# Kernel tuning notes

Measured on AMD Instinct MI355X. Metric: run time of the kernel, lower is better.

## Reference

```python
import jax, jax.numpy as jnp
import numpy as np

N = 50000   # nodes
E = 600000  # edges
D = 128     # emb_dim
L = 3       # num_layers
G = 500     # graphs in batch
AV = 128    # atom feature vocab per column (9 columns)
BV = 8      # bond feature vocab per column (3 columns)


def setup_inputs() -> dict:
    key = jax.random.key(0)
    ks = jax.random.split(key, 16)
    r = lambda k, sh: jax.random.normal(k, sh, jnp.float32) * 0.02
    return dict(
        x=jax.random.randint(ks[0], (N, 9), 0, AV),
        edge_index=jax.random.randint(ks[1], (2, E), 0, N),
        edge_attr=jax.random.randint(ks[2], (E, 3), 0, BV),
        batch=(jnp.arange(N) * G) // N,  # sorted node->graph map, covers all G graphs
        atom_emb=r(ks[3], (9, AV, D)),
        bond_emb=r(ks[4], (L, 3, BV, D)),  # per-layer BondEncoder
        eps=jnp.zeros((L,), jnp.float32),
        conv_w1=r(ks[5], (L, D, 2 * D)), conv_b1=jnp.zeros((L, 2 * D), jnp.float32),
        conv_bn_g=jnp.ones((L, 2 * D), jnp.float32), conv_bn_b=jnp.zeros((L, 2 * D), jnp.float32),
        conv_w2=r(ks[6], (L, 2 * D, D)), conv_b2=jnp.zeros((L, D), jnp.float32),
        bn_g=jnp.ones((L, D), jnp.float32), bn_b=jnp.zeros((L, D), jnp.float32),
        vn_emb=jnp.zeros((1, D), jnp.float32),  # init constant 0, as in torch code
        vn_w1=r(ks[7], (L - 1, D, 2 * D)), vn_b1=jnp.zeros((L - 1, 2 * D), jnp.float32),
        vn_bn1_g=jnp.ones((L - 1, 2 * D), jnp.float32), vn_bn1_b=jnp.zeros((L - 1, 2 * D), jnp.float32),
        vn_w2=r(ks[8], (L - 1, 2 * D, D)), vn_b2=jnp.zeros((L - 1, D), jnp.float32),
        vn_bn2_g=jnp.ones((L - 1, D), jnp.float32), vn_bn2_b=jnp.zeros((L - 1, D), jnp.float32),
    )


def _bn(h, g, b):
    # BatchNorm1d, training-mode batch statistics (biased var), eps=1e-5
    mu = h.mean(0)
    var = h.var(0)
    return (h - mu) * jax.lax.rsqrt(var + 1e-5) * g + b


def reference(x, edge_index, edge_attr, batch, atom_emb, bond_emb, eps,
              conv_w1, conv_b1, conv_bn_g, conv_bn_b, conv_w2, conv_b2,
              bn_g, bn_b, vn_emb, vn_w1, vn_b1, vn_bn1_g, vn_bn1_b,
              vn_w2, vn_b2, vn_bn2_g, vn_bn2_b):
    src, dst = edge_index[0], edge_index[1]
    # AtomEncoder: sum of per-column embeddings -> [N, D]
    h = sum(atom_emb[i][x[:, i]] for i in range(9))
    vn = jnp.broadcast_to(vn_emb[0], (G, D))  # virtualnode_embedding(zeros(G))
    for l in range(L):
        h = h + vn[batch]                                   # virtual-node broadcast
        ee = sum(bond_emb[l, i][edge_attr[:, i]] for i in range(3))  # BondEncoder [E, D]
        msg = jax.nn.relu(h[src] + ee)                      # message: relu(x_j + edge_attr)
        agg = jax.ops.segment_sum(msg, dst, num_segments=N)  # aggr='add'
        t = (1.0 + eps[l]) * h + agg
        t = _bn(t @ conv_w1[l] + conv_b1[l], conv_bn_g[l], conv_bn_b[l])
        t = jax.nn.relu(t) @ conv_w2[l] + conv_b2[l]
        hn = _bn(t, bn_g[l], bn_b[l])                       # outer batch_norms[layer]
        if l < L - 1:
            hn = jax.nn.relu(hn)                            # relu before dropout (non-final)
            # virtual node update: global_add_pool(h_list[layer]) + vn -> MLP
            vt = jax.ops.segment_sum(h, batch, num_segments=G) + vn
            vt = jax.nn.relu(_bn(vt @ vn_w1[l] + vn_b1[l], vn_bn1_g[l], vn_bn1_b[l]))
            vn = jax.nn.relu(_bn(vt @ vn_w2[l] + vn_b2[l], vn_bn2_g[l], vn_bn2_b[l]))
        h = hn
    return h
```

## Files before the change

### kernel.cpp

```cpp
#include <hip/hip_runtime.h>

#define DEV __global__ __launch_bounds__(256)

constexpr int NN = 50000;
constexpr int NE = 600000;
constexpr int D  = 128;
constexpr int NG = 500;
constexpr int NL = 3;
constexpr int SCAN_B = 512;
constexpr int NBLK = (NN + SCAN_B - 1) / SCAN_B;

typedef __attribute__((ext_vector_type(8))) short bf16x8;
typedef __attribute__((ext_vector_type(4))) float f32x4;

__device__ inline ushort f2bf(float f) {
  unsigned u = __builtin_bit_cast(unsigned, f);
  unsigned r = u + 0x7FFFu + ((u >> 16) & 1u);
  return (ushort)(r >> 16);
}
__device__ inline float bf2f(ushort h) {
  unsigned u = ((unsigned)h) << 16;
  return __builtin_bit_cast(float, u);
}


DEV void k_atom(const int* __restrict__ x, const float* __restrict__ emb,
                const float* __restrict__ vne, float* __restrict__ hv) {
  int t = blockIdx.x * 256 + threadIdx.x;
  int n = t >> 5, c = (t & 31) * 4;
  if (n >= NN) return;
  float4 acc = *(const float4*)(vne + c);
  #pragma unroll
  for (int i = 0; i < 9; ++i) {
    int v = x[n * 9 + i];
    float4 e = *(const float4*)(emb + ((size_t)(i * 128 + v)) * D + c);
    acc.x += e.x; acc.y += e.y; acc.z += e.z; acc.w += e.w;
  }
  *(float4*)(hv + (size_t)n * D + c) = acc;
}

DEV void k_vninit(const float* __restrict__ src, float* __restrict__ vn) {
  int t = blockIdx.x * 256 + threadIdx.x;
  int g = t >> 5, c = (t & 31) * 4;
  if (g >= NG) return;
  *(float4*)(vn + (size_t)g * D + c) = *(const float4*)(src + c);
}

DEV void k_post(const float* __restrict__ z, const float* __restrict__ sum,
                const float* __restrict__ sq, const float* __restrict__ gam,
                const float* __restrict__ bet, float invM,
                const float* __restrict__ vnadd, const int* __restrict__ batch,
                float* __restrict__ dst, int M, int relu) {
  int t = blockIdx.x * 256 + threadIdx.x;
  int n = t >> 5, c = (t & 31) * 4;
  if (n >= M) return;
  f32x4 s = *(const f32x4*)(sum + c);
  f32x4 q = *(const f32x4*)(sq + c);
  f32x4 g = *(const f32x4*)(gam + c);
  f32x4 b = *(const f32x4*)(bet + c);
  f32x4 v = *(const f32x4*)(z + (size_t)n * 128 + c);
  f32x4 o;
  #pragma unroll
  for (int j = 0; j < 4; ++j) {
    float mu = s[j] * invM;
    float var = q[j] * invM - mu * mu;
    float sc = g[j] * rsqrtf(var + 1e-5f);
    float sh = b[j] - mu * sc;
    o[j] = fmaf(v[j], sc, sh);
    if (relu) o[j] = fmaxf(o[j], 0.f);
  }
  if (vnadd) {
    f32x4 a = *(const f32x4*)(vnadd + (size_t)batch[n] * 128 + c);
    #pragma unroll
    for (int j = 0; j < 4; ++j) o[j] += a[j];
  }
  *(f32x4*)(dst + (size_t)n * 128 + c) = o;
}


DEV void k_hist(const int* __restrict__ ei, int* __restrict__ cnt) {
  int e = blockIdx.x * 256 + threadIdx.x;
  if (e < NE) atomicAdd(&cnt[ei[NE + e]], 1);
}

__global__ __launch_bounds__(SCAN_B) void k_scan_a(const int* __restrict__ cnt,
                                                   int* __restrict__ rowptr,
                                                   int* __restrict__ bsum) {
  __shared__ int sh[SCAN_B];
  int i = blockIdx.x * SCAN_B + threadIdx.x;
  int v = (i < NN) ? cnt[i] : 0;
  sh[threadIdx.x] = v;
  __syncthreads();
  for (int off = 1; off < SCAN_B; off <<= 1) {
    int u = (threadIdx.x >= (unsigned)off) ? sh[threadIdx.x - off] : 0;
    __syncthreads();
    sh[threadIdx.x] += u;
    __syncthreads();
  }
  if (i < NN) rowptr[i + 1] = sh[threadIdx.x];
  if (threadIdx.x == SCAN_B - 1) bsum[blockIdx.x] = sh[SCAN_B - 1];
}

__global__ void k_scan_b(int* __restrict__ bsum, int nb) {
  if (threadIdx.x == 0 && blockIdx.x == 0) {
    int acc = 0;
    for (int i = 0; i < nb; ++i) { int v = bsum[i]; bsum[i] = acc; acc += v; }
  }
}

__global__ __launch_bounds__(SCAN_B) void k_scan_c(int* __restrict__ rowptr,
                                                   const int* __restrict__ bsum) {
  int i = blockIdx.x * SCAN_B + threadIdx.x;
  if (i < NN) rowptr[i + 1] += bsum[blockIdx.x];
  if (i == 0) rowptr[0] = 0;
}

DEV void k_fill(const int* __restrict__ ei, const int* __restrict__ eattr,
                int* __restrict__ cursor, unsigned* __restrict__ csr) {
  int e = blockIdx.x * 256 + threadIdx.x;
  if (e >= NE) return;
  int dn = ei[NE + e];
  int p = atomicAdd(&cursor[dn], 1);
  unsigned a0 = (unsigned)eattr[e * 3 + 0];
  unsigned a1 = (unsigned)eattr[e * 3 + 1];
  unsigned a2 = (unsigned)eattr[e * 3 + 2];
  csr[p] = (unsigned)ei[e] | (a0 << 17) | (a1 << 20) | (a2 << 23);
}


DEV void k_agg(const float* __restrict__ hv, const unsigned* __restrict__ csr,
               const int* __restrict__ rowptr, const float* __restrict__ bond,
               const float* __restrict__ epsp, unsigned* __restrict__ Ahi,
               unsigned* __restrict__ Alo) {
  __shared__ float eb[3 * 8 * D];
  for (int i = threadIdx.x; i < 3 * 8 * D; i += 256) eb[i] = bond[i];
  __syncthreads();
  int wid = (blockIdx.x * 256 + threadIdx.x) >> 6;
  int lane = threadIdx.x & 63;
  if (wid >= NN) return;
  int d0 = lane * 2;
  float ax = 0.f, ay = 0.f;
  int p = rowptr[wid];
  const int p1 = rowptr[wid + 1];
  for (; p + 4 <= p1; p += 4) {
    unsigned pk[4];
    #pragma unroll
    for (int j = 0; j < 4; ++j) pk[j] = csr[p + j];
    float2 hvv[4];
    #pragma unroll
    for (int j = 0; j < 4; ++j)
      hvv[j] = *(const float2*)(hv + (size_t)(pk[j] & 0x1FFFF) * D + d0);
    #pragma unroll
    for (int j = 0; j < 4; ++j) {
      float2 e0 = *(const float2*)(eb + (((pk[j] >> 17) & 7u)) * D + d0);
      float2 e1 = *(const float2*)(eb + (8 + ((pk[j] >> 20) & 7u)) * D + d0);
      float2 e2 = *(const float2*)(eb + (16 + ((pk[j] >> 23) & 7u)) * D + d0);
      ax += fmaxf(hvv[j].x + e0.x + e1.x + e2.x, 0.f);
      ay += fmaxf(hvv[j].y + e0.y + e1.y + e2.y, 0.f);
    }
  }
  for (; p < p1; ++p) {
    unsigned pk = csr[p];
    float2 hvv = *(const float2*)(hv + (size_t)(pk & 0x1FFFF) * D + d0);
    float2 e0 = *(const float2*)(eb + (((pk >> 17) & 7u)) * D + d0);
    float2 e1 = *(const float2*)(eb + (8 + ((pk >> 20) & 7u)) * D + d0);
    float2 e2 = *(const float2*)(eb + (16 + ((pk >> 23) & 7u)) * D + d0);
    ax += fmaxf(hvv.x + e0.x + e1.x + e2.x, 0.f);
    ay += fmaxf(hvv.y + e0.y + e1.y + e2.y, 0.f);
  }
  float2 hvo = *(const float2*)(hv + (size_t)wid * D + d0);
  float ef = 1.f + epsp[0];
  float a0 = fmaf(ef, hvo.x, ax);
  float a1 = fmaf(ef, hvo.y, ay);
  ushort h0 = f2bf(a0), h1 = f2bf(a1);
  ushort l0 = f2bf(a0 - bf2f(h0)), l1 = f2bf(a1 - bf2f(h1));
  Ahi[(size_t)wid * 64 + lane] = (unsigned)h0 | ((unsigned)h1 << 16);
  Alo[(size_t)wid * 64 + lane] = (unsigned)l0 | ((unsigned)l1 << 16);
}

__global__ __launch_bounds__(256) void k_cvtw(const float* __restrict__ src, int K,
                                              int lognc, ushort* __restrict__ th,
                                              ushort* __restrict__ tl) {
  int NC = 1 << lognc;
  size_t base = (size_t)blockIdx.y * K * NC;
  int i = blockIdx.x * 256 + threadIdx.x;
  if (i >= K * NC) return;
  int k = i >> lognc, c = i & (NC - 1);
  float v = src[base + i];
  ushort hi = f2bf(v);
  th[base + (size_t)c * K + k] = hi;
  tl[base + (size_t)c * K + k] = f2bf(v - bf2f(hi));
}

template <int AMODE, int COLS, int NT, bool ATOMIC>
__global__ __launch_bounds__(NT) void k_mgemm(
    int M, int K, const float* __restrict__ A0, const ushort* __restrict__ Ath,
    const ushort* __restrict__ Atl, const float* __restrict__ bnsum,
    const float* __restrict__ bnsq, const float* __restrict__ bngam,
    const float* __restrict__ bnbet, float invPrevM,
    const ushort* __restrict__ Wth, const ushort* __restrict__ Wtl,
    const float* __restrict__ bias, float* __restrict__ Y,
    float* __restrict__ colsum, float* __restrict__ colsq,
    float* __restrict__ partial) {
  constexpr int NWC = COLS / 64;
  __shared__ __align__(16) ushort Ah[4][128][8];
  __shared__ __align__(16) ushort Al[4][128][8];
  __shared__ __align__(16) ushort Bh[4][COLS][8];
  __shared__ __align__(16) ushort Bl[4][COLS][8];
  __shared__ float bnsc[AMODE == 2 ? 256 : 1];
  __shared__ float bnsh[AMODE == 2 ? 256 : 1];
  const int tid = threadIdx.x;
  const int row0 = blockIdx.x * 128;
  const int lane = tid & 63, w = tid >> 6;
  const int wr = w / NWC, wc = w % NWC;
  const int kc = lane >> 4, lr = lane & 15;

  if (AMODE == 2) {
    for (int c = tid; c < K; c += NT) {
      float mu = bnsum[c] * invPrevM;
      float var = bnsq[c] * invPrevM - mu * mu;
      float sc = bngam[c] * rsqrtf(var + 1e-5f);
      bnsc[c] = sc;
      bnsh[c] = bnbet[c] - mu * sc;
    }
    __syncthreads();
  }

  f32x4 acc[4][4] = {};

  for (int k0 = 0; k0 < K; k0 += 32) {
    for (int i = tid; i < 512; i += NT) {
      const int c = i >> 7, r = i & 127;
      const int gk = k0 + c * 8;
      const int gr = row0 + r;
      if (AMODE == 3) {
        uint4 vh = make_uint4(0, 0, 0, 0), vl = make_uint4(0, 0, 0, 0);
        if (gr < M) {
          vh = *(const uint4*)(Ath + (size_t)gr * K + gk);
          vl = *(const uint4*)(Atl + (size_t)gr * K + gk);
        }
        *(uint4*)&Ah[c][r][0] = vh;
        *(uint4*)&Al[c][r][0] = vl;
      } else {
        float v[8];
        if (gr < M) {
          f32x4 a0 = *(const f32x4*)(A0 + (size_t)gr * K + gk);
          f32x4 a1 = *(const f32x4*)(A0 + (size_t)gr * K + gk + 4);
          if (AMODE == 2) {
            f32x4 s0 = *(const f32x4*)&bnsc[gk];
            f32x4 s1 = *(const f32x4*)&bnsc[gk + 4];
            f32x4 t0 = *(const f32x4*)&bnsh[gk];
            f32x4 t1 = *(const f32x4*)&bnsh[gk + 4];
            #pragma unroll
            for (int j = 0; j < 4; ++j) {
              v[j] = fmaxf(fmaf(a0[j], s0[j], t0[j]), 0.f);
              v[4 + j] = fmaxf(fmaf(a1[j], s1[j], t1[j]), 0.f);
            }
          } else {
            #pragma unroll
            for (int j = 0; j < 4; ++j) { v[j] = a0[j]; v[4 + j] = a1[j]; }
          }
        } else {
          #pragma unroll
          for (int j = 0; j < 8; ++j) v[j] = 0.f;
        }
        alignas(16) ushort th[8], tl[8];
        #pragma unroll
        for (int j = 0; j < 8; ++j) {
          ushort hi = f2bf(v[j]);
          th[j] = hi;
          tl[j] = f2bf(v[j] - bf2f(hi));
        }
        *(uint4*)&Ah[c][r][0] = *(const uint4*)th;
        *(uint4*)&Al[c][r][0] = *(const uint4*)tl;
      }
    }
    for (int i = tid; i < COLS * 4; i += NT) {
      const int c = i / COLS, r = i % COLS;
      const int gk = k0 + c * 8;
      *(uint4*)&Bh[c][r][0] = *(const uint4*)(Wth + (size_t)r * K + gk);
      *(uint4*)&Bl[c][r][0] = *(const uint4*)(Wtl + (size_t)r * K + gk);
    }
    __syncthreads();
    bf16x8 bhf[4], blf[4];
    #pragma unroll
    for (int fc = 0; fc < 4; ++fc) {
      bhf[fc] = *(const bf16x8*)&Bh[kc][wc * 64 + fc * 16 + lr][0];
      blf[fc] = *(const bf16x8*)&Bl[kc][wc * 64 + fc * 16 + lr][0];
    }
    #pragma unroll
    for (int fr = 0; fr < 4; ++fr) {
      bf16x8 ahf = *(const bf16x8*)&Ah[kc][wr * 64 + fr * 16 + lr][0];
      bf16x8 alf = *(const bf16x8*)&Al[kc][wr * 64 + fr * 16 + lr][0];
      #pragma unroll
      for (int fc = 0; fc < 4; ++fc) {
        acc[fr][fc] = __builtin_amdgcn_mfma_f32_16x16x32_bf16(ahf, bhf[fc], acc[fr][fc], 0, 0, 0);
        acc[fr][fc] = __builtin_amdgcn_mfma_f32_16x16x32_bf16(alf, bhf[fc], acc[fr][fc], 0, 0, 0);
        acc[fr][fc] = __builtin_amdgcn_mfma_f32_16x16x32_bf16(ahf, blf[fc], acc[fr][fc], 0, 0, 0);
      }
    }
    __syncthreads();
  }

  float* sred = reinterpret_cast<float*>(&Ah[0][0][0]);
  float* qred = sred + 2 * COLS;
  #pragma unroll
  for (int fc = 0; fc < 4; ++fc) {
    const int gc = wc * 64 + fc * 16 + lr;
    const float bb = bias[gc];
    float cs = 0.f, cq = 0.f;
    #pragma unroll
    for (int fr = 0; fr < 4; ++fr) {
      const int rb = row0 + wr * 64 + fr * 16 + kc * 4;
      #pragma unroll
      for (int rg = 0; rg < 4; ++rg) {
        int gr = rb + rg;
        if (gr < M) {
          float v = acc[fr][fc][rg] + bb;
          Y[(size_t)gr * COLS + gc] = v;
          cs += v;
          cq += v * v;
        }
      }
    }
    cs += __shfl_xor(cs, 16); cs += __shfl_xor(cs, 32);
    cq += __shfl_xor(cq, 16); cq += __shfl_xor(cq, 32);
    if (kc == 0) {
      sred[wr * COLS + gc] = cs;
      qred[wr * COLS + gc] = cq;
    }
  }
  __syncthreads();
  for (int c = tid; c < COLS; c += NT) {
    float s = sred[c] + sred[COLS + c];
    float q = qred[c] + qred[COLS + c];
    if (ATOMIC) {
      atomicAdd(&colsum[c], s);
      atomicAdd(&colsq[c], q);
    } else {
      partial[(size_t)blockIdx.x * 2 * COLS + c] = s;
      partial[(size_t)blockIdx.x * 2 * COLS + COLS + c] = q;
    }
  }
}

__global__ __launch_bounds__(256) void k_red(const float* __restrict__ part, int nb,
                                             int width, float* __restrict__ outSum,
                                             float* __restrict__ outSq) {
  const int j = blockIdx.x;
  float a = 0.f;
  for (int b = threadIdx.x; b < nb; b += 256)
    a += part[(size_t)b * 2 * width + j];
  a += __shfl_xor(a, 1);  a += __shfl_xor(a, 2);  a += __shfl_xor(a, 4);
  a += __shfl_xor(a, 8);  a += __shfl_xor(a, 16); a += __shfl_xor(a, 32);
  __shared__ float red[4];
  const int lane = threadIdx.x & 63, wv = threadIdx.x >> 6;
  if (lane == 0) red[wv] = a;
  __syncthreads();
  if (threadIdx.x == 0) {
    float s = red[0] + red[1] + red[2] + red[3];
    if (j < width) outSum[j] = s;
    else outSq[j - width] = s;
  }
}


DEV void k_pool(const float* __restrict__ hv, const int* __restrict__ batch,
                const float* __restrict__ vn, float* __restrict__ vt) {
  int g = blockIdx.x;
  int lo = 0, hi = NN;
  while (lo < hi) { int mid = (lo + hi) >> 1; if (batch[mid] < g) lo = mid + 1; else hi = mid; }
  int s = lo;
  hi = NN;
  while (lo < hi) { int mid = (lo + hi) >> 1; if (batch[mid] < g + 1) lo = mid + 1; else hi = mid; }
  int e = lo;
  int ry = threadIdx.x >> 5, cx = threadIdx.x & 31;
  float4 acc = make_float4(0.f, 0.f, 0.f, 0.f);
  for (int n = s + ry; n < e; n += 8) {
    float4 v = *(const float4*)(hv + (size_t)n * D + cx * 4);
    acc.x += v.x; acc.y += v.y; acc.z += v.z; acc.w += v.w;
  }
  __shared__ float4 red[8][32];
  red[ry][cx] = acc;
  __syncthreads();
  for (int st = 4; st >= 1; st >>= 1) {
    if (ry < st) {
      float4 o = red[ry + st][cx];
      red[ry][cx].x += o.x; red[ry][cx].y += o.y;
      red[ry][cx].z += o.z; red[ry][cx].w += o.w;
    }
    __syncthreads();
  }
  if (ry == 0) {
    float4 v = red[0][cx];
    float4 b = *(const float4*)(vn + (size_t)g * D + cx * 4);
    v.x += b.x; v.y += b.y; v.z += b.z; v.w += b.w;
    *(float4*)(vt + (size_t)g * D + cx * 4) = v;
  }
}


extern "C" void kernel_launch(void* const* d_in, const int* in_sizes, int n_in,
                              void* d_out, int out_size, void* d_ws, size_t ws_size,
                              hipStream_t stream) {
  const int* x = (const int*)d_in[0];
  const int* ei = (const int*)d_in[1];
  const int* eattr = (const int*)d_in[2];
  const int* batch = (const int*)d_in[3];
  const float* atom_emb = (const float*)d_in[4];
  const float* bond_emb = (const float*)d_in[5];
  const float* eps = (const float*)d_in[6];
  const float* conv_w1 = (const float*)d_in[7];
  const float* conv_b1 = (const float*)d_in[8];
  const float* conv_bn_g = (const float*)d_in[9];
  const float* conv_bn_b = (const float*)d_in[10];
  const float* conv_w2 = (const float*)d_in[11];
  const float* conv_b2 = (const float*)d_in[12];
  const float* bn_g = (const float*)d_in[13];
  const float* bn_b = (const float*)d_in[14];
  const float* vn_emb = (const float*)d_in[15];
  const float* vn_w1 = (const float*)d_in[16];
  const float* vn_b1 = (const float*)d_in[17];
  const float* vn_bn1_g = (const float*)d_in[18];
  const float* vn_bn1_b = (const float*)d_in[19];
  const float* vn_w2 = (const float*)d_in[20];
  const float* vn_b2 = (const float*)d_in[21];
  const float* vn_bn2_g = (const float*)d_in[22];
  const float* vn_bn2_b = (const float*)d_in[23];
  float* out = (float*)d_out;

  char* w = (char*)d_ws;
  auto alloc = [&](size_t bytes) {
    char* p = w;
    w += (bytes + 255) & ~((size_t)255);
    return p;
  };
  float* h   = (float*)alloc((size_t)NN * D * 4);
  float* hv  = (float*)alloc((size_t)NN * D * 4);
  float* y   = (float*)alloc((size_t)NN * 256 * 4);
  unsigned* Ahi = (unsigned*)alloc((size_t)NN * 64 * 4);
  unsigned* Alo = (unsigned*)alloc((size_t)NN * 64 * 4);
  float* vn  = (float*)alloc((size_t)NG * D * 4);
  float* vt  = (float*)alloc((size_t)NG * D * 4);
  float* yv  = (float*)alloc((size_t)NG * 256 * 4);
  float* zv  = (float*)alloc((size_t)NG * D * 4);
  float* stats = (float*)alloc(16 * 512 * 4);
  auto SUM = [&](int slot) { return stats + slot * 512; };
  auto SQ  = [&](int slot) { return stats + slot * 512 + 256; };
  const int gx = (NN + 127) / 128;
  const int gv = (NG + 127) / 128;
  float* partA = (float*)alloc((size_t)gx * 512 * 4);
  float* partB = (float*)alloc((size_t)gx * 256 * 4);
  int* cnt = (int*)alloc((size_t)NN * 4);
  int* rowptr = (int*)alloc((size_t)(NN + 1) * 4);
  int* cursor = (int*)alloc((size_t)NN * 4);
  unsigned* csr = (unsigned*)alloc((size_t)NE * 4);
  int* bsum = (int*)alloc(128 * 4);
  ushort* wt1h = (ushort*)alloc((size_t)NL * 256 * 128 * 2);
  ushort* wt1l = (ushort*)alloc((size_t)NL * 256 * 128 * 2);
  ushort* wt2h = (ushort*)alloc((size_t)NL * 128 * 256 * 2);
  ushort* wt2l = (ushort*)alloc((size_t)NL * 128 * 256 * 2);
  ushort* vw1h = (ushort*)alloc((size_t)2 * 256 * 128 * 2);
  ushort* vw1l = (ushort*)alloc((size_t)2 * 256 * 128 * 2);
  ushort* vw2h = (ushort*)alloc((size_t)2 * 128 * 256 * 2);
  ushort* vw2l = (ushort*)alloc((size_t)2 * 128 * 256 * 2);

  hipMemsetAsync(stats, 0, 16 * 512 * 4, stream);

  k_cvtw<<<dim3(128, NL), 256, 0, stream>>>(conv_w1, 128, 8, wt1h, wt1l);
  k_cvtw<<<dim3(128, NL), 256, 0, stream>>>(conv_w2, 256, 7, wt2h, wt2l);
  k_cvtw<<<dim3(128, 2), 256, 0, stream>>>(vn_w1, 128, 8, vw1h, vw1l);
  k_cvtw<<<dim3(128, 2), 256, 0, stream>>>(vn_w2, 256, 7, vw2h, vw2l);

  k_atom<<<(NN * 32 + 255) / 256, 256, 0, stream>>>(x, atom_emb, vn_emb, hv);
  k_vninit<<<(NG * 32 + 255) / 256, 256, 0, stream>>>(vn_emb, vn);

  hipMemsetAsync(cnt, 0, (size_t)NN * 4, stream);
  k_hist<<<(NE + 255) / 256, 256, 0, stream>>>(ei, cnt);
  k_scan_a<<<NBLK, SCAN_B, 0, stream>>>(cnt, rowptr, bsum);
  k_scan_b<<<1, 64, 0, stream>>>(bsum, NBLK);
  k_scan_c<<<NBLK, SCAN_B, 0, stream>>>(rowptr, bsum);
  hipMemcpyAsync(cursor, rowptr, (size_t)NN * 4, hipMemcpyDeviceToDevice, stream);
  k_fill<<<(NE + 255) / 256, 256, 0, stream>>>(ei, eattr, cursor, csr);

  for (int l = 0; l < NL; ++l) {
    const int sc1 = l, sc2 = 3 + l, sv1 = 6 + l, sv2 = 8 + l;
    k_agg<<<(NN * 64 + 255) / 256, 256, 0, stream>>>(
        hv, csr, rowptr, bond_emb + (size_t)l * 3 * 8 * D, eps + l, Ahi, Alo);

    k_mgemm<3, 256, 512, false><<<gx, 512, 0, stream>>>(
        NN, 128, nullptr, (const ushort*)Ahi, (const ushort*)Alo,
        nullptr, nullptr, nullptr, nullptr, 0.f,
        wt1h + (size_t)l * 256 * 128, wt1l + (size_t)l * 256 * 128,
        conv_b1 + l * 256, y, nullptr, nullptr, partA);
    k_red<<<512, 256, 0, stream>>>(partA, gx, 256, SUM(sc1), SQ(sc1));
    k_mgemm<2, 128, 256, false><<<gx, 256, 0, stream>>>(
        NN, 256, y, nullptr, nullptr, SUM(sc1), SQ(sc1),
        conv_bn_g + l * 256, conv_bn_b + l * 256, 1.f / NN,
        wt2h + (size_t)l * 128 * 256, wt2l + (size_t)l * 128 * 256,
        conv_b2 + l * 128, h, nullptr, nullptr, partB);
    k_red<<<256, 256, 0, stream>>>(partB, gx, 128, SUM(sc2), SQ(sc2));

    if (l < NL - 1) {
      k_pool<<<NG, 256, 0, stream>>>(hv, batch, vn, vt);
      k_mgemm<0, 256, 512, true><<<gv, 512, 0, stream>>>(
          NG, 128, vt, nullptr, nullptr, nullptr, nullptr, nullptr, nullptr, 0.f,
          vw1h + (size_t)l * 256 * 128, vw1l + (size_t)l * 256 * 128,
          vn_b1 + l * 256, yv, SUM(sv1), SQ(sv1), nullptr);
      k_mgemm<2, 128, 256, true><<<gv, 256, 0, stream>>>(
          NG, 256, yv, nullptr, nullptr, SUM(sv1), SQ(sv1),
          vn_bn1_g + l * 256, vn_bn1_b + l * 256, 1.f / NG,
          vw2h + (size_t)l * 128 * 256, vw2l + (size_t)l * 128 * 256,
          vn_b2 + l * 128, zv, SUM(sv2), SQ(sv2), nullptr);
      k_post<<<(NG * 32 + 255) / 256, 256, 0, stream>>>(
          zv, SUM(sv2), SQ(sv2), vn_bn2_g + l * 128, vn_bn2_b + l * 128,
          1.f / NG, nullptr, nullptr, vn, NG, 1);
      k_post<<<(NN * 32 + 255) / 256, 256, 0, stream>>>(
          h, SUM(sc2), SQ(sc2), bn_g + l * 128, bn_b + l * 128,
          1.f / NN, vn, batch, hv, NN, 1);
    } else {
      k_post<<<(NN * 32 + 255) / 256, 256, 0, stream>>>(
          h, SUM(sc2), SQ(sc2), bn_g + l * 128, bn_b + l * 128,
          1.f / NN, nullptr, nullptr, out, NN, 0);
    }
  }
}
```

Measured before the change: 824.5 us.

## Store first GEMM output in bf16 and merge small setup kernels

```diff
diff --git a/kernel.cpp b/kernel.cpp
--- a/kernel.cpp
+++ b/kernel.cpp
@@ -24,8 +24,17 @@
 }
 
 
-DEV void k_atom(const int* __restrict__ x, const float* __restrict__ emb,
-                const float* __restrict__ vne, float* __restrict__ hv) {
+constexpr int NB_ATOM = (NN * 32 + 255) / 256;
+constexpr int NB_VNI  = (NG * 32 + 255) / 256;
+DEV void k_atomvn(const int* __restrict__ x, const float* __restrict__ emb,
+                  const float* __restrict__ vne, float* __restrict__ hv,
+                  float* __restrict__ vn) {
+  if ((int)blockIdx.x >= NB_ATOM) {
+    int t = (blockIdx.x - NB_ATOM) * 256 + threadIdx.x;
+    int g = t >> 5, c = (t & 31) * 4;
+    if (g < NG) *(float4*)(vn + (size_t)g * D + c) = *(const float4*)(vne + c);
+    return;
+  }
   int t = blockIdx.x * 256 + threadIdx.x;
   int n = t >> 5, c = (t & 31) * 4;
   if (n >= NN) return;
@@ -37,13 +46,6 @@
     acc.x += e.x; acc.y += e.y; acc.z += e.z; acc.w += e.w;
   }
   *(float4*)(hv + (size_t)n * D + c) = acc;
-}
-
-DEV void k_vninit(const float* __restrict__ src, float* __restrict__ vn) {
-  int t = blockIdx.x * 256 + threadIdx.x;
-  int g = t >> 5, c = (t & 31) * 4;
-  if (g >= NG) return;
-  *(float4*)(vn + (size_t)g * D + c) = *(const float4*)(src + c);
 }
 
 DEV void k_post(const float* __restrict__ z, const float* __restrict__ sum,
@@ -101,17 +103,17 @@
   if (threadIdx.x == SCAN_B - 1) bsum[blockIdx.x] = sh[SCAN_B - 1];
 }
 
-__global__ void k_scan_b(int* __restrict__ bsum, int nb) {
-  if (threadIdx.x == 0 && blockIdx.x == 0) {
-    int acc = 0;
-    for (int i = 0; i < nb; ++i) { int v = bsum[i]; bsum[i] = acc; acc += v; }
-  }
-}
-
 __global__ __launch_bounds__(SCAN_B) void k_scan_c(int* __restrict__ rowptr,
                                                    const int* __restrict__ bsum) {
+  __shared__ int off;
+  if (threadIdx.x == 0) {
+    int a = 0;
+    for (int b = 0; b < (int)blockIdx.x; ++b) a += bsum[b];
+    off = a;
+  }
+  __syncthreads();
   int i = blockIdx.x * SCAN_B + threadIdx.x;
-  if (i < NN) rowptr[i + 1] += bsum[blockIdx.x];
+  if (i < NN) rowptr[i + 1] += off;
   if (i == 0) rowptr[0] = 0;
 }
 
@@ -178,30 +180,39 @@
   Alo[(size_t)wid * 64 + lane] = (unsigned)l0 | ((unsigned)l1 << 16);
 }
 
-__global__ __launch_bounds__(256) void k_cvtw(const float* __restrict__ src, int K,
-                                              int lognc, ushort* __restrict__ th,
-                                              ushort* __restrict__ tl) {
-  int NC = 1 << lognc;
-  size_t base = (size_t)blockIdx.y * K * NC;
+__global__ __launch_bounds__(256) void k_cvtw_all(
+    const float* __restrict__ w1, const float* __restrict__ w2,
+    const float* __restrict__ v1, const float* __restrict__ v2,
+    ushort* __restrict__ t1h, ushort* __restrict__ t1l,
+    ushort* __restrict__ t2h, ushort* __restrict__ t2l,
+    ushort* __restrict__ u1h, ushort* __restrict__ u1l,
+    ushort* __restrict__ u2h, ushort* __restrict__ u2l) {
+  int seg = blockIdx.y;
+  const float* src; ushort *th, *tl; int K, lognc, idx;
+  if (seg < 3)      { src = w1; th = t1h; tl = t1l; K = 128; lognc = 8; idx = seg; }
+  else if (seg < 6) { src = w2; th = t2h; tl = t2l; K = 256; lognc = 7; idx = seg - 3; }
+  else if (seg < 8) { src = v1; th = u1h; tl = u1l; K = 128; lognc = 8; idx = seg - 6; }
+  else              { src = v2; th = u2h; tl = u2l; K = 256; lognc = 7; idx = seg - 8; }
+  size_t base = (size_t)idx * (K << lognc);
   int i = blockIdx.x * 256 + threadIdx.x;
-  if (i >= K * NC) return;
-  int k = i >> lognc, c = i & (NC - 1);
+  if (i >= (K << lognc)) return;
+  int k = i >> lognc, c = i & ((1 << lognc) - 1);
   float v = src[base + i];
   ushort hi = f2bf(v);
   th[base + (size_t)c * K + k] = hi;
   tl[base + (size_t)c * K + k] = f2bf(v - bf2f(hi));
 }
 
-template <int AMODE, int COLS, int NT, bool ATOMIC>
+template <int AMODE, int COLS, int NT, bool ATOMIC, bool OUTBF>
 __global__ __launch_bounds__(NT) void k_mgemm(
-    int M, int K, const float* __restrict__ A0, const ushort* __restrict__ Ath,
-    const ushort* __restrict__ Atl, const float* __restrict__ bnsum,
+    int M, int K, const float* __restrict__ A0, const ushort* __restrict__ Abh,
+    const ushort* __restrict__ Abl, const float* __restrict__ bnsum,
     const float* __restrict__ bnsq, const float* __restrict__ bngam,
     const float* __restrict__ bnbet, float invPrevM,
     const ushort* __restrict__ Wth, const ushort* __restrict__ Wtl,
-    const float* __restrict__ bias, float* __restrict__ Y,
-    float* __restrict__ colsum, float* __restrict__ colsq,
-    float* __restrict__ partial) {
+    const float* __restrict__ bias, float* __restrict__ Yf,
+    ushort* __restrict__ Yb, float* __restrict__ colsum,
+    float* __restrict__ colsq, float* __restrict__ partial) {
   constexpr int NWC = COLS / 64;
   __shared__ __align__(16) ushort Ah[4][128][8];
   __shared__ __align__(16) ushort Al[4][128][8];
@@ -236,27 +247,23 @@
       if (AMODE == 3) {
         uint4 vh = make_uint4(0, 0, 0, 0), vl = make_uint4(0, 0, 0, 0);
         if (gr < M) {
-          vh = *(const uint4*)(Ath + (size_t)gr * K + gk);
-          vl = *(const uint4*)(Atl + (size_t)gr * K + gk);
+          vh = *(const uint4*)(Abh + (size_t)gr * K + gk);
+          vl = *(const uint4*)(Abl + (size_t)gr * K + gk);
         }
         *(uint4*)&Ah[c][r][0] = vh;
         *(uint4*)&Al[c][r][0] = vl;
       } else {
         float v[8];
         if (gr < M) {
-          f32x4 a0 = *(const f32x4*)(A0 + (size_t)gr * K + gk);
-          f32x4 a1 = *(const f32x4*)(A0 + (size_t)gr * K + gk + 4);
           if (AMODE == 2) {
-            f32x4 s0 = *(const f32x4*)&bnsc[gk];
-            f32x4 s1 = *(const f32x4*)&bnsc[gk + 4];
-            f32x4 t0 = *(const f32x4*)&bnsh[gk];
-            f32x4 t1 = *(const f32x4*)&bnsh[gk + 4];
+            alignas(16) ushort yq[8];
+            *(uint4*)yq = *(const uint4*)(Abh + (size_t)gr * K + gk);
             #pragma unroll
-            for (int j = 0; j < 4; ++j) {
-              v[j] = fmaxf(fmaf(a0[j], s0[j], t0[j]), 0.f);
-              v[4 + j] = fmaxf(fmaf(a1[j], s1[j], t1[j]), 0.f);
-            }
+            for (int j = 0; j < 8; ++j)
+              v[j] = fmaxf(fmaf(bf2f(yq[j]), bnsc[gk + j], bnsh[gk + j]), 0.f);
           } else {
+            f32x4 a0 = *(const f32x4*)(A0 + (size_t)gr * K + gk);
+            f32x4 a1 = *(const f32x4*)(A0 + (size_t)gr * K + gk + 4);
             #pragma unroll
             for (int j = 0; j < 4; ++j) { v[j] = a0[j]; v[4 + j] = a1[j]; }
           }
@@ -317,7 +324,8 @@
         int gr = rb + rg;
         if (gr < M) {
           float v = acc[fr][fc][rg] + bb;
-          Y[(size_t)gr * COLS + gc] = v;
+          if (OUTBF) Yb[(size_t)gr * COLS + gc] = f2bf(v);
+          else       Yf[(size_t)gr * COLS + gc] = v;
           cs += v;
           cq += v * v;
         }
@@ -437,12 +445,12 @@
   };
   float* h   = (float*)alloc((size_t)NN * D * 4);
   float* hv  = (float*)alloc((size_t)NN * D * 4);
-  float* y   = (float*)alloc((size_t)NN * 256 * 4);
+  ushort* y  = (ushort*)alloc((size_t)NN * 256 * 2);
   unsigned* Ahi = (unsigned*)alloc((size_t)NN * 64 * 4);
   unsigned* Alo = (unsigned*)alloc((size_t)NN * 64 * 4);
   float* vn  = (float*)alloc((size_t)NG * D * 4);
   float* vt  = (float*)alloc((size_t)NG * D * 4);
-  float* yv  = (float*)alloc((size_t)NG * 256 * 4);
+  ushort* yv = (ushort*)alloc((size_t)NG * 256 * 2);
   float* zv  = (float*)alloc((size_t)NG * D * 4);
   float* stats = (float*)alloc(16 * 512 * 4);
   auto SUM = [&](int slot) { return stats + slot * 512; };
@@ -467,20 +475,17 @@
 
   hipMemsetAsync(stats, 0, 16 * 512 * 4, stream);
 
-  k_cvtw<<<dim3(128, NL), 256, 0, stream>>>(conv_w1, 128, 8, wt1h, wt1l);
-  k_cvtw<<<dim3(128, NL), 256, 0, stream>>>(conv_w2, 256, 7, wt2h, wt2l);
-  k_cvtw<<<dim3(128, 2), 256, 0, stream>>>(vn_w1, 128, 8, vw1h, vw1l);
-  k_cvtw<<<dim3(128, 2), 256, 0, stream>>>(vn_w2, 256, 7, vw2h, vw2l);
-
-  k_atom<<<(NN * 32 + 255) / 256, 256, 0, stream>>>(x, atom_emb, vn_emb, hv);
-  k_vninit<<<(NG * 32 + 255) / 256, 256, 0, stream>>>(vn_emb, vn);
+  k_cvtw_all<<<dim3(128, 10), 256, 0, stream>>>(
+      conv_w1, conv_w2, vn_w1, vn_w2, wt1h, wt1l, wt2h, wt2l,
+      vw1h, vw1l, vw2h, vw2l);
+
+  k_atomvn<<<NB_ATOM + NB_VNI, 256, 0, stream>>>(x, atom_emb, vn_emb, hv, vn);
 
   hipMemsetAsync(cnt, 0, (size_t)NN * 4, stream);
   k_hist<<<(NE + 255) / 256, 256, 0, stream>>>(ei, cnt);
   k_scan_a<<<NBLK, SCAN_B, 0, stream>>>(cnt, rowptr, bsum);
-  k_scan_b<<<1, 64, 0, stream>>>(bsum, NBLK);
   k_scan_c<<<NBLK, SCAN_B, 0, stream>>>(rowptr, bsum);
-  hipMemcpyAsync(cursor, rowptr, (size_t)NN * 4, hipMemcpyDeviceToDevice, stream);
+  (void)hipMemcpyAsync(cursor, rowptr, (size_t)NN * 4, hipMemcpyDeviceToDevice, stream);
   k_fill<<<(NE + 255) / 256, 256, 0, stream>>>(ei, eattr, cursor, csr);
 
   for (int l = 0; l < NL; ++l) {
@@ -488,30 +493,30 @@
     k_agg<<<(NN * 64 + 255) / 256, 256, 0, stream>>>(
         hv, csr, rowptr, bond_emb + (size_t)l * 3 * 8 * D, eps + l, Ahi, Alo);
 
-    k_mgemm<3, 256, 512, false><<<gx, 512, 0, stream>>>(
+    k_mgemm<3, 256, 512, false, true><<<gx, 512, 0, stream>>>(
         NN, 128, nullptr, (const ushort*)Ahi, (const ushort*)Alo,
         nullptr, nullptr, nullptr, nullptr, 0.f,
         wt1h + (size_t)l * 256 * 128, wt1l + (size_t)l * 256 * 128,
-        conv_b1 + l * 256, y, nullptr, nullptr, partA);
+        conv_b1 + l * 256, nullptr, y, nullptr, nullptr, partA);
     k_red<<<512, 256, 0, stream>>>(partA, gx, 256, SUM(sc1), SQ(sc1));
-    k_mgemm<2, 128, 256, false><<<gx, 256, 0, stream>>>(
-        NN, 256, y, nullptr, nullptr, SUM(sc1), SQ(sc1),
+    k_mgemm<2, 128, 256, false, false><<<gx, 256, 0, stream>>>(
+        NN, 256, nullptr, y, nullptr, SUM(sc1), SQ(sc1),
         conv_bn_g + l * 256, conv_bn_b + l * 256, 1.f / NN,
         wt2h + (size_t)l * 128 * 256, wt2l + (size_t)l * 128 * 256,
-        conv_b2 + l * 128, h, nullptr, nullptr, partB);
+        conv_b2 + l * 128, h, nullptr, nullptr, nullptr, partB);
     k_red<<<256, 256, 0, stream>>>(partB, gx, 128, SUM(sc2), SQ(sc2));
 
     if (l < NL - 1) {
       k_pool<<<NG, 256, 0, stream>>>(hv, batch, vn, vt);
-      k_mgemm<0, 256, 512, true><<<gv, 512, 0, stream>>>(
+      k_mgemm<0, 256, 512, true, true><<<gv, 512, 0, stream>>>(
           NG, 128, vt, nullptr, nullptr, nullptr, nullptr, nullptr, nullptr, 0.f,
           vw1h + (size_t)l * 256 * 128, vw1l + (size_t)l * 256 * 128,
-          vn_b1 + l * 256, yv, SUM(sv1), SQ(sv1), nullptr);
-      k_mgemm<2, 128, 256, true><<<gv, 256, 0, stream>>>(
-          NG, 256, yv, nullptr, nullptr, SUM(sv1), SQ(sv1),
+          vn_b1 + l * 256, nullptr, yv, SUM(sv1), SQ(sv1), nullptr);
+      k_mgemm<2, 128, 256, true, false><<<gv, 256, 0, stream>>>(
+          NG, 256, nullptr, yv, nullptr, SUM(sv1), SQ(sv1),
           vn_bn1_g + l * 256, vn_bn1_b + l * 256, 1.f / NG,
           vw2h + (size_t)l * 128 * 256, vw2l + (size_t)l * 128 * 256,
-          vn_b2 + l * 128, zv, SUM(sv2), SQ(sv2), nullptr);
+          vn_b2 + l * 128, zv, nullptr, SUM(sv2), SQ(sv2), nullptr);
       k_post<<<(NG * 32 + 255) / 256, 256, 0, stream>>>(
           zv, SUM(sv2), SQ(sv2), vn_bn2_g + l * 128, vn_bn2_b + l * 128,
           1.f / NG, nullptr, nullptr, vn, NG, 1);
```

Result: faster. 793.9 us (-3.7%).
